# Optimization experiments

Hardware: AMD Instinct MI355X
Metric: run time of the kernel (lower is better)

## Reference

```python
import jax, jax.numpy as jnp
import numpy as np


def _axis_taps(g, size):
    # g: continuous grid coordinate; returns two neighbor indices (clamped)
    # and their linear interpolation weights, matching the HDRNet CUDA kernel:
    #   w = max(1 - |i + 0.5 - g|, 0)
    f = jnp.floor(g - 0.5)
    taps = []
    for off in (0.0, 1.0):
        idx = f + off
        w = jnp.maximum(1.0 - jnp.abs(idx + 0.5 - g), 0.0)
        i = jnp.clip(idx, 0, size - 1).astype(jnp.int32)
        taps.append((i, w))
    return taps


def bilateral_slice_apply(grid, guide, inp):
    # grid: [B, gh, gw, gd, n_out*(n_in+1)]   (has_offset=True)
    # guide: [B, H, W] in [0,1]
    # inp:  [B, H, W, n_in]
    B, gh, gw, gd, nc = grid.shape
    _, H, W, n_in = inp.shape
    n_out = nc // (n_in + 1)

    # continuous grid coords for each pixel / guide value
    gx = (jnp.arange(W, dtype=grid.dtype) + 0.5) * (gw / W)   # [W]
    gy = (jnp.arange(H, dtype=grid.dtype) + 0.5) * (gh / H)   # [H]
    gz = guide * gd                                           # [B,H,W]

    x_taps = _axis_taps(gx, gw)   # idx/w: [W]
    y_taps = _axis_taps(gy, gh)   # idx/w: [H]
    z_taps = _axis_taps(gz, gd)   # idx/w: [B,H,W]

    b = jnp.arange(B)[:, None, None]
    coeff = jnp.zeros((B, H, W, nc), dtype=grid.dtype)
    for yi, wy in y_taps:
        for xi, wx in x_taps:
            for zi, wz in z_taps:
                g = grid[b, yi[None, :, None], xi[None, None, :], zi]  # [B,H,W,nc]
                w = (wy[None, :, None] * wx[None, None, :] * wz)[..., None]
                coeff = coeff + w * g

    # per-pixel affine apply: out_o = sum_i A[o,i]*in_i + A[o,n_in]
    coeff = coeff.reshape(B, H, W, n_out, n_in + 1)
    out = jnp.einsum('bhwoc,bhwc->bhwo', coeff[..., :n_in], inp) + coeff[..., n_in]
    return out


def setup_inputs() -> dict:
    key = jax.random.key(0)
    k1, k2, k3 = jax.random.split(key, 3)
    B, gh, gw, gd = 4, 16, 16, 8
    H, W, n_in, n_out = 1024, 1024, 3, 3
    nc = n_out * (n_in + 1)  # has_offset=True -> 12
    grid = jax.random.normal(k1, (B, gh, gw, gd, nc), dtype=jnp.float32)
    guide = jax.random.uniform(k2, (B, H, W), dtype=jnp.float32)
    inp = jax.random.normal(k3, (B, H, W, n_in), dtype=jnp.float32)
    return {"grid": grid, "guide": guide, "input": inp}


def reference(grid, guide, input):
    return bilateral_slice_apply(grid, guide, input)
```

## Files before the change

### kernel.cpp

```cpp
#include <hip/hip_runtime.h>
#include <hip/hip_fp16.h>


struct __align__(16) H2x4 { __half2 x, y, z, w; };
struct __align__(8)  H2x2 { __half2 a, b; };

__global__ __launch_bounds__(256, 6) void BilateralSliceApply_kernel(
    const float* __restrict__ grid,
    const float* __restrict__ guide,
    const float* __restrict__ inp,
    float* __restrict__ out)
{
    __shared__ H2x4 lA[1024];
    __shared__ H2x4 lB[512];

    const int tx = blockIdx.x;
    const int ty = blockIdx.y;
    const int b  = blockIdx.z;
    const int t  = threadIdx.x;
    const int xl = t & 63;

    const int x0 = tx << 6;
    const int y0 = ty << 5;

    const int fy  = (ty == 0) ? -1 : ((ty - 1) >> 1);
    const int ycA = fy < 0 ? 0 : fy;
    const int ycB = (fy + 1 > 15) ? 15 : fy + 1;

    const int fx  = (xl < 32) ? (tx - 1) : tx;
    const int ix0 = fx < 0 ? 0 : fx;
    const int ix1 = (fx + 1 > 15) ? 15 : fx + 1;
    const float wx1 = ((float)(x0 + xl) + 0.5f) * 0.015625f - 0.5f - (float)fx;

    const int bbase = b << 4;
    const int g0grp = t >> 6;
#pragma unroll
    for (int q = 0; q < 4; ++q) {
        const int L  = g0grp + (q << 2);
        const int yc = L >> 3;
        const int z  = L & 7;
        const int ycell = yc ? ycB : ycA;
        const int cb = (bbase + ycell) << 4;
        const float* p0 = grid + (size_t)(((cb + ix0) << 3) + z) * 12;
        const float* p1 = grid + (size_t)(((cb + ix1) << 3) + z) * 12;
        const float4 a0 = *(const float4*)(p0 + 0);
        const float4 a1 = *(const float4*)(p0 + 4);
        const float4 a2 = *(const float4*)(p0 + 8);
        const float4 b0 = *(const float4*)(p1 + 0);
        const float4 b1 = *(const float4*)(p1 + 4);
        const float4 b2 = *(const float4*)(p1 + 8);
        const float v0  = fmaf(wx1, b0.x - a0.x, a0.x);
        const float v1  = fmaf(wx1, b0.y - a0.y, a0.y);
        const float v2  = fmaf(wx1, b0.z - a0.z, a0.z);
        const float v3  = fmaf(wx1, b0.w - a0.w, a0.w);
        const float v4  = fmaf(wx1, b1.x - a1.x, a1.x);
        const float v5  = fmaf(wx1, b1.y - a1.y, a1.y);
        const float v6  = fmaf(wx1, b1.z - a1.z, a1.z);
        const float v7  = fmaf(wx1, b1.w - a1.w, a1.w);
        const float v8  = fmaf(wx1, b2.x - a2.x, a2.x);
        const float v9  = fmaf(wx1, b2.y - a2.y, a2.y);
        const float v10 = fmaf(wx1, b2.z - a2.z, a2.z);
        const float v11 = fmaf(wx1, b2.w - a2.w, a2.w);

        H2x4 rowA;
        rowA.x = __floats2half2_rn(v0, v1);
        rowA.y = __floats2half2_rn(v2, v3);
        rowA.z = __floats2half2_rn(v4, v5);
        rowA.w = __floats2half2_rn(v6, v7);
        lA[(L << 6) + xl] = rowA;

        H2x2 rowB;
        rowB.a = __floats2half2_rn(v8, v9);
        rowB.b = __floats2half2_rn(v10, v11);
        ((H2x2*)lB)[(((z << 6) + xl) << 1) + yc] = rowB;
    }
    __syncthreads();

    const int r0 = t >> 6;
    for (int k = 0; k < 8; ++k) {
        const int row = r0 + (k << 2);
        const int y   = y0 + row;
        const float wy1 = ((float)y + 0.5f) * 0.015625f - 0.5f - (float)fy;
        const float wy0 = 1.0f - wy1;
        const int pp = (((b << 10) + y) << 10) + x0 + xl;

        const float gz  = guide[pp] * 8.0f;
        const float fz  = floorf(gz - 0.5f);
        const float wz1 = gz - 0.5f - fz;
        const float wz0 = 1.0f - wz1;
        const int ifz = (int)fz;
        const int iz0 = ifz < 0 ? 0 : (ifz > 7 ? 7 : ifz);
        const int nz  = ifz + 1;
        const int iz1 = nz < 0 ? 0 : (nz > 7 ? 7 : nz);

        const __half2 hA0 = __float2half2_rn(wy0 * wz0);
        const __half2 hA1 = __float2half2_rn(wy0 * wz1);
        const __half2 hB0 = __float2half2_rn(wy1 * wz0);
        const __half2 hB1 = __float2half2_rn(wy1 * wz1);

        const H2x4 vA00 = lA[(iz0 << 6) + xl];
        const H2x4 vA01 = lA[(iz1 << 6) + xl];
        const H2x4 vA10 = lA[((8 + iz0) << 6) + xl];
        const H2x4 vA11 = lA[((8 + iz1) << 6) + xl];
        const H2x4 vB0  = lB[(iz0 << 6) + xl];
        const H2x4 vB1  = lB[(iz1 << 6) + xl];

        __half2 q0 = __hmul2(hA0, vA00.x);
        __half2 q1 = __hmul2(hA0, vA00.y);
        __half2 q2 = __hmul2(hA0, vA00.z);
        __half2 q3 = __hmul2(hA0, vA00.w);
        q0 = __hfma2(hA1, vA01.x, q0);
        q1 = __hfma2(hA1, vA01.y, q1);
        q2 = __hfma2(hA1, vA01.z, q2);
        q3 = __hfma2(hA1, vA01.w, q3);
        q0 = __hfma2(hB0, vA10.x, q0);
        q1 = __hfma2(hB0, vA10.y, q1);
        q2 = __hfma2(hB0, vA10.z, q2);
        q3 = __hfma2(hB0, vA10.w, q3);
        q0 = __hfma2(hB1, vA11.x, q0);
        q1 = __hfma2(hB1, vA11.y, q1);
        q2 = __hfma2(hB1, vA11.z, q2);
        q3 = __hfma2(hB1, vA11.w, q3);

        __half2 q4 = __hmul2(hA0, vB0.x);
        __half2 q5 = __hmul2(hA0, vB0.y);
        q4 = __hfma2(hA1, vB1.x, q4);
        q5 = __hfma2(hA1, vB1.y, q5);
        q4 = __hfma2(hB0, vB0.z, q4);
        q5 = __hfma2(hB0, vB0.w, q5);
        q4 = __hfma2(hB1, vB1.z, q4);
        q5 = __hfma2(hB1, vB1.w, q5);

        const float c0  = __low2float(q0),  c1  = __high2float(q0);
        const float c2  = __low2float(q1),  c3  = __high2float(q1);
        const float c4  = __low2float(q2),  c5  = __high2float(q2);
        const float c6  = __low2float(q3),  c7  = __high2float(q3);
        const float c8  = __low2float(q4),  c9  = __high2float(q4);
        const float c10 = __low2float(q5),  c11 = __high2float(q5);

        const float in0 = inp[(size_t)pp * 3 + 0];
        const float in1 = inp[(size_t)pp * 3 + 1];
        const float in2 = inp[(size_t)pp * 3 + 2];

        out[(size_t)pp * 3 + 0] = fmaf(c0, in0, fmaf(c1,  in1, fmaf(c2,  in2, c3)));
        out[(size_t)pp * 3 + 1] = fmaf(c4, in0, fmaf(c5,  in1, fmaf(c6,  in2, c7)));
        out[(size_t)pp * 3 + 2] = fmaf(c8, in0, fmaf(c9,  in1, fmaf(c10, in2, c11)));
    }
}

extern "C" void kernel_launch(void* const* d_in, const int* in_sizes, int n_in,
                              void* d_out, int out_size, void* d_ws, size_t ws_size,
                              hipStream_t stream) {
    const float* grid  = (const float*)d_in[0];
    const float* guide = (const float*)d_in[1];
    const float* inp   = (const float*)d_in[2];
    float* out = (float*)d_out;

    dim3 gridDim(16, 32, 4);
    BilateralSliceApply_kernel<<<gridDim, 256, 0, stream>>>(grid, guide, inp, out);
}
```

Before: 117.6 us.

## Prefetch guide and input before grid staging, apply affine in half2

Each thread now loads all eight of its guide and input values into registers before the grid-staging phase and barrier, so those global loads overlap the grid fetch and LDS fill. The per-pixel affine apply is done with packed half2 multiplies on the input, followed by a horizontal add, and the output is written as a float3 store. Launch bounds drop from 6 to 4 blocks per SM to leave room for the extra registers. This trades occupancy and fp16 precision on the input values and output products for fewer dependent load stalls and fewer scalar ops.

```diff
diff --git a/kernel.cpp b/kernel.cpp
--- a/kernel.cpp
+++ b/kernel.cpp
@@ -5,7 +5,7 @@
 struct __align__(16) H2x4 { __half2 x, y, z, w; };
 struct __align__(8)  H2x2 { __half2 a, b; };
 
-__global__ __launch_bounds__(256, 6) void BilateralSliceApply_kernel(
+__global__ __launch_bounds__(256, 4) void BilateralSliceApply_kernel(
     const float* __restrict__ grid,
     const float* __restrict__ guide,
     const float* __restrict__ inp,
@@ -34,6 +34,18 @@
 
     const int bbase = b << 4;
     const int g0grp = t >> 6;
+
+    const int r0 = t >> 6;
+    const int pp0 = (((b << 10) + y0 + r0) << 10) + x0 + xl;
+    float  gz8[8];
+    float3 in8[8];
+#pragma unroll
+    for (int k = 0; k < 8; ++k) {
+        const int pp = pp0 + (k << 12);
+        gz8[k] = guide[pp];
+        in8[k] = *(const float3*)(inp + (size_t)pp * 3);
+    }
+
 #pragma unroll
     for (int q = 0; q < 4; ++q) {
         const int L  = g0grp + (q << 2);
@@ -76,15 +88,15 @@
     }
     __syncthreads();
 
-    const int r0 = t >> 6;
+#pragma unroll
     for (int k = 0; k < 8; ++k) {
         const int row = r0 + (k << 2);
         const int y   = y0 + row;
         const float wy1 = ((float)y + 0.5f) * 0.015625f - 0.5f - (float)fy;
         const float wy0 = 1.0f - wy1;
-        const int pp = (((b << 10) + y) << 10) + x0 + xl;
+        const int pp = pp0 + (k << 12);
 
-        const float gz  = guide[pp] * 8.0f;
+        const float gz  = gz8[k] * 8.0f;
         const float fz  = floorf(gz - 0.5f);
         const float wz1 = gz - 0.5f - fz;
         const float wz0 = 1.0f - wz1;
@@ -131,20 +143,19 @@
         q4 = __hfma2(hB1, vB1.z, q4);
         q5 = __hfma2(hB1, vB1.w, q5);
 
-        const float c0  = __low2float(q0),  c1  = __high2float(q0);
-        const float c2  = __low2float(q1),  c3  = __high2float(q1);
-        const float c4  = __low2float(q2),  c5  = __high2float(q2);
-        const float c6  = __low2float(q3),  c7  = __high2float(q3);
-        const float c8  = __low2float(q4),  c9  = __high2float(q4);
-        const float c10 = __low2float(q5),  c11 = __high2float(q5);
+        const float3 in = in8[k];
+        const __half2 i01 = __floats2half2_rn(in.x, in.y);
+        const __half2 i21 = __floats2half2_rn(in.z, 1.0f);
 
-        const float in0 = inp[(size_t)pp * 3 + 0];
-        const float in1 = inp[(size_t)pp * 3 + 1];
-        const float in2 = inp[(size_t)pp * 3 + 2];
+        __half2 r0h = __hmul2(q0, i01); r0h = __hfma2(q1, i21, r0h);
+        __half2 r1h = __hmul2(q2, i01); r1h = __hfma2(q3, i21, r1h);
+        __half2 r2h = __hmul2(q4, i01); r2h = __hfma2(q5, i21, r2h);
 
-        out[(size_t)pp * 3 + 0] = fmaf(c0, in0, fmaf(c1,  in1, fmaf(c2,  in2, c3)));
-        out[(size_t)pp * 3 + 1] = fmaf(c4, in0, fmaf(c5,  in1, fmaf(c6,  in2, c7)));
-        out[(size_t)pp * 3 + 2] = fmaf(c8, in0, fmaf(c9,  in1, fmaf(c10, in2, c11)));
+        float3 o;
+        o.x = __low2float(r0h) + __high2float(r0h);
+        o.y = __low2float(r1h) + __high2float(r1h);
+        o.z = __low2float(r2h) + __high2float(r2h);
+        *(float3*)(out + (size_t)pp * 3) = o;
     }
 }
 
```

Measured after the change: 115.9 us. No clear change (-1.4%).
